# Kernel optimization log

Measured on AMD Instinct MI355X. Metric: run time of the kernel, lower is better.

Reference implementation:

```python
import jax, jax.numpy as jnp
import numpy as np

H = 16          # query heads
KV = 8          # kv heads
D = 256         # head_dim
HID = 3584      # hidden_size
ROPE_BASE = 10000.0
SCALING = 256.0 ** -0.5          # query_pre_attn_scalar ** -0.5
SOFTCAP = 50.0                   # attn_logit_softcapping
WINDOW = 1536 - 1                # sliding_window - 1 (layer_idx 0 is even)


def _rope_neox(x, positions):
    # x: [T, nh, D]; neox style: rotate the two halves of the head dim
    half = D // 2
    inv_freq = 1.0 / (ROPE_BASE ** (jnp.arange(0, D, 2, dtype=jnp.float32) / D))  # [half]
    freqs = positions.astype(jnp.float32)[:, None] * inv_freq[None, :]            # [T, half]
    cos = jnp.cos(freqs)[:, None, :]  # [T, 1, half]
    sin = jnp.sin(freqs)[:, None, :]
    x1, x2 = x[..., :half], x[..., half:]
    return jnp.concatenate([x1 * cos - x2 * sin, x2 * cos + x1 * sin], axis=-1)


def setup_inputs() -> dict:
    key = jax.random.key(0)
    k1, k2, k3 = jax.random.split(key, 3)
    T = 3072
    hidden_states = jax.random.normal(k1, (T, HID), dtype=jnp.float32)
    w_qkv = jax.random.normal(k2, (H * D + 2 * KV * D, HID), dtype=jnp.float32) * 0.02
    w_o = jax.random.normal(k3, (HID, H * D), dtype=jnp.float32) * 0.02
    positions = jnp.arange(T, dtype=jnp.int64)
    return {"positions": positions, "hidden_states": hidden_states,
            "w_qkv": w_qkv, "w_o": w_o}


def reference(positions, hidden_states, w_qkv, w_o):
    T = hidden_states.shape[0]
    qkv = hidden_states @ w_qkv.T                       # [T, (H+2KV)*D]
    q, k, v = jnp.split(qkv, [H * D, H * D + KV * D], axis=-1)
    q = q.reshape(T, H, D)
    k = k.reshape(T, KV, D)
    v = v.reshape(T, KV, D)
    q = _rope_neox(q, positions)
    k = _rope_neox(k, positions)
    # GQA: repeat kv heads (2 query heads per kv head)
    k = jnp.repeat(k, H // KV, axis=1)                  # [T, H, D]
    v = jnp.repeat(v, H // KV, axis=1)
    scores = jnp.einsum('thd,shd->hts', q, k) * SCALING  # [H, T, T]
    scores = SOFTCAP * jnp.tanh(scores / SOFTCAP)       # logit softcapping
    i = positions[:, None]
    j = positions[None, :]
    mask = (j <= i) & (i - j <= WINDOW)                 # causal + sliding window
    scores = jnp.where(mask[None, :, :], scores, -jnp.inf)
    probs = jax.nn.softmax(scores, axis=-1)
    attn = jnp.einsum('hts,shd->thd', probs, v).reshape(T, H * D)
    return attn @ w_o.T                                 # [T, HID]
```

## Files before the change

### kernel.cpp

```cpp
#include <hip/hip_runtime.h>
#include <math.h>

typedef unsigned short u16;
typedef __attribute__((ext_vector_type(8))) short short8;
typedef __attribute__((ext_vector_type(4))) float f32x4;
typedef __attribute__((ext_vector_type(4))) unsigned short u16x4;

#define HN 16
#define KVH 8
#define DH 256
#define HID 3584
#define T_LEN 3072
#define QKV_N 8192
#define O_N 4096
#define WIN 1535
#define SCALING 0.0625f
#define SOFTCAP 50.0f
#define KOFF 4096
#define VOFF 6144
#define PSTR 72
#define NJT 48
#define M_FIX 20.0f

__device__ __forceinline__ u16 f2bf(float f) {
  unsigned u = __float_as_uint(f);
  u += 0x7FFFu + ((u >> 16) & 1u);
  return (u16)(u >> 16);
}
__device__ __forceinline__ float bf2f(u16 b) {
  return __uint_as_float(((unsigned)b) << 16);
}

__device__ __forceinline__ void gload_lds16(const void* g, void* l) {
  __builtin_amdgcn_global_load_lds(
      (const __attribute__((address_space(1))) void*)g,
      (__attribute__((address_space(3))) void*)l, 16, 0, 0);
}

__device__ __forceinline__ f32x4 mfma_bf16(short8 a, short8 b, f32x4 c) {
  return __builtin_amdgcn_mfma_f32_16x16x32_bf16(a, b, c, 0, 0, 0);
}

#define BARX()                                  \
  do {                                          \
    __builtin_amdgcn_sched_barrier(0);          \
    __builtin_amdgcn_s_barrier();               \
    __builtin_amdgcn_sched_barrier(0);          \
  } while (0)

__global__ __launch_bounds__(256) void cvt_kernel(const float* __restrict__ in,
                                                  u16* __restrict__ out, int n) {
  int i = (blockIdx.x * 256 + threadIdx.x) * 4;
  if (i >= n) return;
  float4 v = *(const float4*)(in + i);
  u16x4 o;
  o[0] = f2bf(v.x); o[1] = f2bf(v.y); o[2] = f2bf(v.z); o[3] = f2bf(v.w);
  *(u16x4*)(out + i) = o;
}

template <int OUT_BF16>
__global__ __launch_bounds__(512, 2) void gemm8p(const u16* __restrict__ A,
                                                 const u16* __restrict__ B,
                                                 void* __restrict__ Cv,
                                                 int N, int K, int ntn, int cpx) {
  __shared__ u16 sA[2][256 * 64];
  __shared__ u16 sB[2][256 * 64];

  const int bid = blockIdx.x;
  const int wg = (bid & 7) * cpx + (bid >> 3);
  const int bm = wg / ntn, bn = wg % ntn;
  const int row0 = bm * 256, col0 = bn * 256;
  const int tid = threadIdx.x, lane = tid & 63, wid = tid >> 6;
  const int wr = wid >> 2, wc = wid & 3;
  const int NT = K >> 6;

  const int srow = lane >> 3;
  const int sg = (lane & 7) ^ srow;

  auto stage = [&](int tau, int kind) {
    if (tau >= NT) return;
    const int b = tau & 1;
    const int rbase = (kind & 1) * 128;
    const u16* src;
    u16* dst;
    if (kind >= 2) {
      src = A + (size_t)(row0 + rbase + wid * 8 + srow) * K + (size_t)tau * 64 + sg * 8;
      dst = &sA[b][(rbase + wid * 8) * 64];
    } else {
      src = B + (size_t)(col0 + rbase + wid * 8 + srow) * K + (size_t)tau * 64 + sg * 8;
      dst = &sB[b][(rbase + wid * 8) * 64];
    }
    gload_lds16(src, dst);
    gload_lds16(src + (size_t)64 * K, dst + 64 * 64);
  };

  f32x4 acc[8][4] = {};
  const int fr = lane & 15;
  const int fh = fr & 7;
  const int gk0 = (lane >> 4) ^ fh;
  const int gk1 = ((lane >> 4) + 4) ^ fh;

  stage(0, 0); stage(0, 1); stage(0, 2); stage(0, 3);
  stage(1, 0); stage(1, 1); stage(1, 2);
  __builtin_amdgcn_sched_barrier(0);
  asm volatile("s_waitcnt vmcnt(6)" ::: "memory");
  BARX();

  for (int u = 0; u < NT; ++u) {
    const int b = u & 1;
    const u16* pA = &sA[b][0];
    const u16* pB = &sB[b][0];
    short8 bf[4][2], afA[2][2], afB[2][2];

#define LDB_(ni, kk) (*(const short8*)&pB[(wc * 64 + (ni)*16 + fr) * 64 + (kk ? gk1 : gk0) * 8])
#define LDA_(mi, kk) (*(const short8*)&pA[(wr * 128 + (mi)*16 + fr) * 64 + (kk ? gk1 : gk0) * 8])
#define MFMA2(AF, mi0)                                                   \
  __builtin_amdgcn_s_setprio(1);                                        \
  _Pragma("unroll") for (int ni = 0; ni < 4; ++ni) {                    \
    acc[mi0][ni] = mfma_bf16(AF[0][0], bf[ni][0], acc[mi0][ni]);        \
    acc[mi0][ni] = mfma_bf16(AF[0][1], bf[ni][1], acc[mi0][ni]);        \
    acc[mi0 + 1][ni] = mfma_bf16(AF[1][0], bf[ni][0], acc[mi0 + 1][ni]);\
    acc[mi0 + 1][ni] = mfma_bf16(AF[1][1], bf[ni][1], acc[mi0 + 1][ni]);\
  }                                                                      \
  __builtin_amdgcn_s_setprio(0);                                        \
  asm volatile("s_waitcnt lgkmcnt(0)" ::: "memory");

#pragma unroll
    for (int ni = 0; ni < 4; ++ni) { bf[ni][0] = LDB_(ni, 0); bf[ni][1] = LDB_(ni, 1); }
    afA[0][0] = LDA_(0, 0); afA[0][1] = LDA_(0, 1);
    afA[1][0] = LDA_(1, 0); afA[1][1] = LDA_(1, 1);
    stage(u + 1, 3);
    BARX();
    MFMA2(afA, 0);
    BARX();
    afA[0][0] = LDA_(2, 0); afA[0][1] = LDA_(2, 1);
    afA[1][0] = LDA_(3, 0); afA[1][1] = LDA_(3, 1);
    stage(u + 2, 0);
    BARX();
    MFMA2(afA, 2);
    BARX();
    afA[0][0] = LDA_(4, 0); afA[0][1] = LDA_(4, 1);
    afA[1][0] = LDA_(5, 0); afA[1][1] = LDA_(5, 1);
    afB[0][0] = LDA_(6, 0); afB[0][1] = LDA_(6, 1);
    afB[1][0] = LDA_(7, 0); afB[1][1] = LDA_(7, 1);
    stage(u + 2, 1);
    BARX();
    MFMA2(afA, 4);
    BARX();
    stage(u + 2, 2);
    __builtin_amdgcn_sched_barrier(0);
    if (u + 2 < NT) {
      asm volatile("s_waitcnt vmcnt(6)" ::: "memory");
    } else {
      asm volatile("s_waitcnt vmcnt(0)" ::: "memory");
    }
    BARX();
    MFMA2(afB, 6);
    BARX();
#undef LDB_
#undef LDA_
#undef MFMA2
  }

#pragma unroll
  for (int mi = 0; mi < 8; ++mi) {
#pragma unroll
    for (int ni = 0; ni < 4; ++ni) {
      const int r = row0 + wr * 128 + mi * 16 + (lane >> 4) * 4;
      const int c = col0 + wc * 64 + ni * 16 + (lane & 15);
#pragma unroll
      for (int j = 0; j < 4; ++j) {
        float v = acc[mi][ni][j];
        if (OUT_BF16)
          ((u16*)Cv)[(size_t)(r + j) * N + c] = f2bf(v);
        else
          ((float*)Cv)[(size_t)(r + j) * N + c] = v;
      }
    }
  }
}

__global__ __launch_bounds__(256) void rope_kernel(u16* __restrict__ qkv) {
  int idx = blockIdx.x * 256 + threadIdx.x;
  int d = idx & 127;
  int hh = (idx >> 7) % 24;
  int t = idx / (24 * 128);
  if (t >= T_LEN) return;
  size_t base = (size_t)t * QKV_N + (hh < HN ? hh * DH : HN * DH + (hh - HN) * DH);
  float inv = exp2f((float)d * (-13.287712379549449f / 128.0f));
  float ang = (float)t * inv;
  float s = sinf(ang), c = cosf(ang);
  float x1 = bf2f(qkv[base + d]);
  float x2 = bf2f(qkv[base + d + 128]);
  qkv[base + d] = f2bf(x1 * c - x2 * s);
  qkv[base + d + 128] = f2bf(x2 * c + x1 * s);
}

__global__ __launch_bounds__(256) void vtrans_kernel(const u16* __restrict__ qkv,
                                                     u16* __restrict__ vt) {
  __shared__ u16 tile[256 * 72];
  const int jb = blockIdx.x * 64;
  const int kvh = blockIdx.y;
  const int tid = threadIdx.x;
  const int t = tid & 63, dc = tid >> 6;

  const u16* src = qkv + (size_t)(jb + t) * QKV_N + VOFF + kvh * DH + dc * 64;
#pragma unroll
  for (int i = 0; i < 8; ++i) {
    short8 v = *(const short8*)(src + i * 8);
    int d0 = dc * 64 + i * 8;
#pragma unroll
    for (int j = 0; j < 8; ++j) tile[(d0 + j) * 72 + t] = (u16)(short)v[j];
  }
  __syncthreads();

  u16* dst = vt + ((size_t)kvh * NJT + blockIdx.x) * 16384;
#pragma unroll
  for (int s = 0; s < 8; ++s) {
    int G = s * 256 + tid;
    int d = G >> 3, g = G & 7;
    short8 x = *(const short8*)&tile[d * 72 + ((g ^ (d & 7)) * 8)];
    *(short8*)(dst + G * 8) = x;
  }
}

__global__ __launch_bounds__(256) void attn_kernel(const u16* __restrict__ qkv,
                                                   const u16* __restrict__ vt,
                                                   u16* __restrict__ po,
                                                   float* __restrict__ ml) {
  const int wg = blockIdx.x;
  const int kvh = wg & 7;
  const int rest = wg >> 3;
  const int qt = rest >> 2;
  const int c = (rest >> 1) & 1;
  const int h = kvh * 2 + (rest & 1);
  const int qb = qt * 64;
  const int tid = threadIdx.x, lane = tid & 63, w = tid >> 6;

  __shared__ u16 sK[64 * 256];
  __shared__ u16 sVt[64 * 256];
  __shared__ u16 sP[4][16 * PSTR];

  int jmin = qb - WIN; if (jmin < 0) jmin = 0;
  const int jt0 = jmin >> 6, jt1 = qb >> 6;
  const int nt = jt1 - jt0 + 1;
  const int half = (nt + 1) >> 1;
  const int t_beg = (c == 0) ? jt0 : jt0 + half;
  const int t_end = (c == 0) ? jt0 + half : jt1 + 1;

  const int qrow = qb + w * 16 + (lane & 15);
  short8 qf[8];
  {
    const u16* qp = qkv + (size_t)qrow * QKV_N + h * DH + (lane >> 4) * 8;
#pragma unroll
    for (int kc = 0; kc < 8; ++kc) qf[kc] = *(const short8*)(qp + kc * 32);
  }

  f32x4 O[16];
#pragma unroll
  for (int i = 0; i < 16; ++i) O[i] = f32x4{0.f, 0.f, 0.f, 0.f};
  float lrow[4] = {0.f, 0.f, 0.f, 0.f};

  const int dl = lane & 15;
  const int vb0 = dl * 64 + (((lane >> 4)) ^ (dl & 7)) * 8;
  const int vb1 = dl * 64 + (((lane >> 4) + 4) ^ (dl & 7)) * 8;

  for (int jt = t_beg; jt < t_end; ++jt) {
    const int jb = jt * 64;
#pragma unroll
    for (int i = 0; i < 8; ++i) {
      int rl = w * 16 + i * 2 + (lane >> 5);
      int g = (lane & 31) ^ (rl & 7);
      gload_lds16(qkv + (size_t)(jb + rl) * QKV_N + KOFF + kvh * DH + g * 8,
                  &sK[(w * 16 + i * 2) * 256]);
    }
    {
      const u16* vtile = vt + ((size_t)kvh * NJT + jt) * 16384;
#pragma unroll
      for (int s = 0; s < 8; ++s) {
        int id = w * 8 + s;
        gload_lds16(vtile + id * 512 + lane * 8, &sVt[id * 512]);
      }
    }
    __syncthreads();

    f32x4 S[4];
#pragma unroll
    for (int nf = 0; nf < 4; ++nf) S[nf] = f32x4{0.f, 0.f, 0.f, 0.f};
#pragma unroll
    for (int nf = 0; nf < 4; ++nf) {
      int krow = nf * 16 + (lane & 15);
#pragma unroll
      for (int kc = 0; kc < 8; ++kc) {
        int g = (kc * 4 + (lane >> 4)) ^ (krow & 7);
        short8 kf = *(const short8*)&sK[krow * 256 + g * 8];
        S[nf] = mfma_bf16(qf[kc], kf, S[nf]);
      }
    }

#pragma unroll
    for (int r = 0; r < 4; ++r) {
      const int irow = qb + w * 16 + (lane >> 4) * 4 + r;
      const int ql = (lane >> 4) * 4 + r;
#pragma unroll
      for (int nf = 0; nf < 4; ++nf) {
        int j = jb + nf * 16 + (lane & 15);
        float x = S[nf][r] * (SCALING / SOFTCAP);
        float e2 = __expf(-2.0f * fabsf(x));
        float th = (1.0f - e2) / (1.0f + e2);
        th = x >= 0.0f ? th : -th;
        float val = SOFTCAP * th;
        bool ok = (j <= irow) && (irow - j <= WIN);
        float p = ok ? __expf(val - M_FIX) : 0.0f;
        lrow[r] += p;
        sP[w][ql * PSTR + nf * 16 + (lane & 15)] = f2bf(p);
      }
    }

    short8 pf0 = *(const short8*)&sP[w][(lane & 15) * PSTR + (lane >> 4) * 8];
    short8 pf1 = *(const short8*)&sP[w][(lane & 15) * PSTR + 32 + (lane >> 4) * 8];
#pragma unroll
    for (int nf = 0; nf < 16; ++nf) {
      short8 vf0 = *(const short8*)&sVt[nf * 1024 + vb0];
      short8 vf1 = *(const short8*)&sVt[nf * 1024 + vb1];
      O[nf] = mfma_bf16(pf0, vf0, O[nf]);
      O[nf] = mfma_bf16(pf1, vf1, O[nf]);
    }
    __syncthreads();
  }

#pragma unroll
  for (int r = 0; r < 4; ++r) {
#pragma unroll
    for (int off = 8; off >= 1; off >>= 1) lrow[r] += __shfl_xor(lrow[r], off);
  }

#pragma unroll
  for (int nf = 0; nf < 16; ++nf) {
    int d = nf * 16 + (lane & 15);
#pragma unroll
    for (int r = 0; r < 4; ++r) {
      int trow = qb + w * 16 + (lane >> 4) * 4 + r;
      po[(((size_t)c * T_LEN + trow) * HN + h) * DH + d] = f2bf(O[nf][r]);
    }
  }
  if ((lane & 15) == 0) {
#pragma unroll
    for (int r = 0; r < 4; ++r) {
      int trow = qb + w * 16 + (lane >> 4) * 4 + r;
      size_t mi = (((size_t)c * T_LEN + trow) * HN + h) * 2;
      ml[mi] = M_FIX;
      ml[mi + 1] = lrow[r];
    }
  }
}

__global__ __launch_bounds__(256) void combine_kernel(const u16* __restrict__ po,
                                                      const float* __restrict__ ml,
                                                      u16* __restrict__ attnb) {
  const int t = blockIdx.x;
  const int h = threadIdx.x >> 4;
  const int d0 = (threadIdx.x & 15) * 16;
  const size_t row = (size_t)t * HN + h;
  const float l0 = ml[row * 2 + 1];
  const float l1 = ml[(size_t)T_LEN * HN * 2 + row * 2 + 1];
  const float inv = 1.0f / (l0 + l1);
  const size_t i0 = row * DH + d0;
  const size_t i1 = (size_t)T_LEN * HN * DH + i0;
#pragma unroll
  for (int half = 0; half < 2; ++half) {
    short8 x0 = *(const short8*)(po + i0 + half * 8);
    short8 x1 = *(const short8*)(po + i1 + half * 8);
    short8 o;
#pragma unroll
    for (int j = 0; j < 8; ++j)
      o[j] = (short)f2bf((bf2f((u16)x0[j]) + bf2f((u16)x1[j])) * inv);
    *(short8*)(attnb + i0 + half * 8) = o;
  }
}

extern "C" void kernel_launch(void* const* d_in, const int* in_sizes, int n_in,
                              void* d_out, int out_size, void* d_ws, size_t ws_size,
                              hipStream_t stream) {
  const float* hidden = (const float*)d_in[1];
  const float* w_qkv = (const float*)d_in[2];
  const float* w_o = (const float*)d_in[3];
  float* out = (float*)d_out;
  char* ws = (char*)d_ws;

  u16* wqkvb = (u16*)(ws);
  u16* po = (u16*)(ws);
  float* ml = (float*)(ws + 50331648);
  u16* attnb = (u16*)(ws);
  u16* hb = (u16*)(ws + 58720256);
  u16* vtb = (u16*)(ws + 58720256);
  u16* qkvb = (u16*)(ws + 80740352);
  u16* wob = (u16*)(ws + 80740352);

  {
    int n = T_LEN * HID;
    cvt_kernel<<<dim3((n / 4 + 255) / 256), 256, 0, stream>>>(hidden, hb, n);
  }
  {
    int n = QKV_N * HID;
    cvt_kernel<<<dim3((n / 4 + 255) / 256), 256, 0, stream>>>(w_qkv, wqkvb, n);
  }
  gemm8p<1><<<dim3(384), 512, 0, stream>>>(hb, wqkvb, qkvb, QKV_N, HID, 32, 48);
  {
    int n = T_LEN * 24 * 128;
    rope_kernel<<<dim3(n / 256), 256, 0, stream>>>(qkvb);
  }
  vtrans_kernel<<<dim3(NJT, KVH), 256, 0, stream>>>(qkvb, vtb);
  attn_kernel<<<dim3(1536), 256, 0, stream>>>(qkvb, vtb, po, ml);
  {
    int n = HID * O_N;
    cvt_kernel<<<dim3((n / 4 + 255) / 256), 256, 0, stream>>>(w_o, wob, n);
  }
  combine_kernel<<<dim3(T_LEN), 256, 0, stream>>>(po, ml, attnb);
  gemm8p<0><<<dim3(168), 512, 0, stream>>>(attnb, wob, out, HID, O_N, 14, 21);
}
```

Baseline: 555.4 us.

## Use 32x32x16 MFMA GEMM for output projection and precompute RoPE cos/sin table

Adds a new gemm32 kernel that uses 32x32x16 bf16 MFMA instructions with a 256x256 tile, double-buffered LDS and an interleaved load/compute schedule, and uses it for the final output projection instead of gemm8p. The larger MFMA shape is meant to raise matrix throughput and cut LDS fragment reads per FLOP. RoPE now reads cos/sin from a table built once per call instead of computing sin/cos per element for all 24 heads. The table kernel adds a launch and workspace traffic, and the new GEMM relies on tile sizes dividing the problem.

Result: no change. 563.4 us (+1.4%).

```diff
diff --git a/kernel.cpp b/kernel.cpp
--- a/kernel.cpp
+++ b/kernel.cpp
@@ -4,6 +4,7 @@
 typedef unsigned short u16;
 typedef __attribute__((ext_vector_type(8))) short short8;
 typedef __attribute__((ext_vector_type(4))) float f32x4;
+typedef __attribute__((ext_vector_type(16))) float f32x16;
 typedef __attribute__((ext_vector_type(4))) unsigned short u16x4;
 
 #define HN 16
@@ -40,6 +41,9 @@
 __device__ __forceinline__ f32x4 mfma_bf16(short8 a, short8 b, f32x4 c) {
   return __builtin_amdgcn_mfma_f32_16x16x32_bf16(a, b, c, 0, 0, 0);
 }
+__device__ __forceinline__ f32x16 mfma32_bf16(short8 a, short8 b, f32x16 c) {
+  return __builtin_amdgcn_mfma_f32_32x32x16_bf16(a, b, c, 0, 0, 0);
+}
 
 #define BARX()                                  \
   do {                                          \
@@ -180,20 +184,148 @@
   }
 }
 
-__global__ __launch_bounds__(256) void rope_kernel(u16* __restrict__ qkv) {
+__global__ __launch_bounds__(512, 2) void gemm32(const u16* __restrict__ A,
+                                                 const u16* __restrict__ B,
+                                                 float* __restrict__ C,
+                                                 int N, int K, int ntn, int cpx) {
+  __shared__ u16 sA[2][256 * 64];
+  __shared__ u16 sB[2][256 * 64];
+
+  const int bid = blockIdx.x;
+  const int wg = (bid & 7) * cpx + (bid >> 3);
+  const int bm = wg / ntn, bn = wg % ntn;
+  const int row0 = bm * 256, col0 = bn * 256;
+  const int tid = threadIdx.x, lane = tid & 63, wid = tid >> 6;
+  const int wr = wid >> 2, wc = wid & 3;
+  const int NT = K >> 6;
+
+  const int srow = lane >> 3;
+  const int sg = (lane & 7) ^ srow;
+
+  auto stage = [&](int tau, int kind) {
+    if (tau >= NT) return;
+    const int b = tau & 1;
+    const int rbase = (kind & 1) * 128;
+    const u16* src;
+    u16* dst;
+    if (kind >= 2) {
+      src = A + (size_t)(row0 + rbase + wid * 8 + srow) * K + (size_t)tau * 64 + sg * 8;
+      dst = &sA[b][(rbase + wid * 8) * 64];
+    } else {
+      src = B + (size_t)(col0 + rbase + wid * 8 + srow) * K + (size_t)tau * 64 + sg * 8;
+      dst = &sB[b][(rbase + wid * 8) * 64];
+    }
+    gload_lds16(src, dst);
+    gload_lds16(src + (size_t)64 * K, dst + 64 * 64);
+  };
+
+  f32x16 acc[4][2] = {};
+  const int fr32 = lane & 31;
+  int gk32[4];
+#pragma unroll
+  for (int kk = 0; kk < 4; ++kk) gk32[kk] = ((kk << 1) | (lane >> 5)) ^ (fr32 & 7);
+
+  stage(0, 0); stage(0, 1); stage(0, 2); stage(0, 3);
+  stage(1, 0); stage(1, 1); stage(1, 2);
+  __builtin_amdgcn_sched_barrier(0);
+  asm volatile("s_waitcnt vmcnt(6)" ::: "memory");
+  BARX();
+
+  for (int u = 0; u < NT; ++u) {
+    const int b = u & 1;
+    const u16* pA = &sA[b][0];
+    const u16* pB = &sB[b][0];
+    short8 bf[2][4], afA[4], afB[4];
+
+#define LDB32_(nt, kk) (*(const short8*)&pB[(wc * 64 + (nt)*32 + fr32) * 64 + gk32[kk] * 8])
+#define LDA32_(mt, kk) (*(const short8*)&pA[(wr * 128 + (mt)*32 + fr32) * 64 + gk32[kk] * 8])
+#define MFMA32X(AF, mt)                                                  \
+  __builtin_amdgcn_s_setprio(1);                                        \
+  _Pragma("unroll") for (int nt = 0; nt < 2; ++nt) {                    \
+    _Pragma("unroll") for (int kk = 0; kk < 4; ++kk)                    \
+      acc[mt][nt] = mfma32_bf16(AF[kk], bf[nt][kk], acc[mt][nt]);       \
+  }                                                                      \
+  __builtin_amdgcn_s_setprio(0);                                        \
+  asm volatile("s_waitcnt lgkmcnt(0)" ::: "memory");
+
+#pragma unroll
+    for (int nt = 0; nt < 2; ++nt)
+#pragma unroll
+      for (int kk = 0; kk < 4; ++kk) bf[nt][kk] = LDB32_(nt, kk);
+#pragma unroll
+    for (int kk = 0; kk < 4; ++kk) afA[kk] = LDA32_(0, kk);
+    stage(u + 1, 3);
+    BARX();
+    MFMA32X(afA, 0);
+    BARX();
+#pragma unroll
+    for (int kk = 0; kk < 4; ++kk) afA[kk] = LDA32_(1, kk);
+    stage(u + 2, 0);
+    BARX();
+    MFMA32X(afA, 1);
+    BARX();
+#pragma unroll
+    for (int kk = 0; kk < 4; ++kk) afA[kk] = LDA32_(2, kk);
+#pragma unroll
+    for (int kk = 0; kk < 4; ++kk) afB[kk] = LDA32_(3, kk);
+    stage(u + 2, 1);
+    BARX();
+    MFMA32X(afA, 2);
+    BARX();
+    stage(u + 2, 2);
+    __builtin_amdgcn_sched_barrier(0);
+    if (u + 2 < NT) {
+      asm volatile("s_waitcnt vmcnt(6)" ::: "memory");
+    } else {
+      asm volatile("s_waitcnt vmcnt(0)" ::: "memory");
+    }
+    BARX();
+    MFMA32X(afB, 3);
+    BARX();
+#undef LDB32_
+#undef LDA32_
+#undef MFMA32X
+  }
+
+#pragma unroll
+  for (int mt = 0; mt < 4; ++mt) {
+#pragma unroll
+    for (int nt = 0; nt < 2; ++nt) {
+      const int c = col0 + wc * 64 + nt * 32 + fr32;
+#pragma unroll
+      for (int reg = 0; reg < 16; ++reg) {
+        const int r = row0 + wr * 128 + mt * 32 + (reg & 3) + 8 * (reg >> 2) + 4 * (lane >> 5);
+        C[(size_t)r * N + c] = acc[mt][nt][reg];
+      }
+    }
+  }
+}
+
+__global__ __launch_bounds__(256) void rope_table_kernel(float* __restrict__ tab) {
+  int idx = blockIdx.x * 256 + threadIdx.x;
+  int d = idx & 127;
+  int t = idx >> 7;
+  float inv = exp2f((float)d * (-13.287712379549449f / 128.0f));
+  float ang = (float)t * inv;
+  float2 cs;
+  cs.x = cosf(ang);
+  cs.y = sinf(ang);
+  *(float2*)(tab + idx * 2) = cs;
+}
+
+__global__ __launch_bounds__(256) void rope_kernel(u16* __restrict__ qkv,
+                                                   const float* __restrict__ tab) {
   int idx = blockIdx.x * 256 + threadIdx.x;
   int d = idx & 127;
   int hh = (idx >> 7) % 24;
   int t = idx / (24 * 128);
   if (t >= T_LEN) return;
   size_t base = (size_t)t * QKV_N + (hh < HN ? hh * DH : HN * DH + (hh - HN) * DH);
-  float inv = exp2f((float)d * (-13.287712379549449f / 128.0f));
-  float ang = (float)t * inv;
-  float s = sinf(ang), c = cosf(ang);
+  float2 cs = *(const float2*)(tab + ((size_t)(t << 7) + d) * 2);
   float x1 = bf2f(qkv[base + d]);
   float x2 = bf2f(qkv[base + d + 128]);
-  qkv[base + d] = f2bf(x1 * c - x2 * s);
-  qkv[base + d + 128] = f2bf(x2 * c + x1 * s);
+  qkv[base + d] = f2bf(x1 * cs.x - x2 * cs.y);
+  qkv[base + d + 128] = f2bf(x2 * cs.x + x1 * cs.y);
 }
 
 __global__ __launch_bounds__(256) void vtrans_kernel(const u16* __restrict__ qkv,
@@ -394,6 +526,7 @@
   u16* attnb = (u16*)(ws);
   u16* hb = (u16*)(ws + 58720256);
   u16* vtb = (u16*)(ws + 58720256);
+  float* ropetab = (float*)(ws + 71303168);
   u16* qkvb = (u16*)(ws + 80740352);
   u16* wob = (u16*)(ws + 80740352);
 
@@ -406,9 +539,10 @@
     cvt_kernel<<<dim3((n / 4 + 255) / 256), 256, 0, stream>>>(w_qkv, wqkvb, n);
   }
   gemm8p<1><<<dim3(384), 512, 0, stream>>>(hb, wqkvb, qkvb, QKV_N, HID, 32, 48);
+  rope_table_kernel<<<dim3(T_LEN * 128 / 256), 256, 0, stream>>>(ropetab);
   {
     int n = T_LEN * 24 * 128;
-    rope_kernel<<<dim3(n / 256), 256, 0, stream>>>(qkvb);
+    rope_kernel<<<dim3(n / 256), 256, 0, stream>>>(qkvb, ropetab);
   }
   vtrans_kernel<<<dim3(NJT, KVH), 256, 0, stream>>>(qkvb, vtb);
   attn_kernel<<<dim3(1536), 256, 0, stream>>>(qkvb, vtb, po, ml);
@@ -417,5 +551,5 @@
     cvt_kernel<<<dim3((n / 4 + 255) / 256), 256, 0, stream>>>(w_o, wob, n);
   }
   combine_kernel<<<dim3(T_LEN), 256, 0, stream>>>(po, ml, attnb);
-  gemm8p<0><<<dim3(168), 512, 0, stream>>>(attnb, wob, out, HID, O_N, 14, 21);
-}
+  gemm32<<<dim3(168), 512, 0, stream>>>(attnb, wob, out, HID, O_N, 14, 21);
+}
```

## Merge conversion kernels and precompute RoPE table in spare GEMM blocks

Applied to the files above, without the earlier changes.

Merges the hidden-state and QKV-weight fp32-to-bf16 conversions into one launch. It also folds the w_o conversion into the combine kernel and adds 128 extra blocks to the QKV GEMM launch that build a cos/sin table for RoPE, stored temporarily in the output buffer. The rope kernel then reads that table instead of calling sin/cos itself. This cuts launch count and transcendental work, at the cost of extra table traffic and heavier combine blocks. The combine kernel also gains a multiply by 1.0 that does nothing.

Result: faster. 534.3 us (-3.8%).

```diff
diff --git a/kernel.cpp b/kernel.cpp
--- a/kernel.cpp
+++ b/kernel.cpp
@@ -48,29 +48,61 @@
     __builtin_amdgcn_sched_barrier(0);          \
   } while (0)
 
-__global__ __launch_bounds__(256) void cvt_kernel(const float* __restrict__ in,
-                                                  u16* __restrict__ out, int n) {
-  int i = (blockIdx.x * 256 + threadIdx.x) * 4;
-  if (i >= n) return;
-  float4 v = *(const float4*)(in + i);
+__global__ __launch_bounds__(256) void cvt2_kernel(const float* __restrict__ a,
+                                                   u16* __restrict__ da, int nva,
+                                                   const float* __restrict__ b,
+                                                   u16* __restrict__ db, int nvb) {
+  int v = blockIdx.x * 256 + threadIdx.x;
+  const float* src;
+  u16* dst;
+  if (v < nva) {
+    src = a + (size_t)v * 4;
+    dst = da + (size_t)v * 4;
+  } else if (v < nva + nvb) {
+    int u = v - nva;
+    src = b + (size_t)u * 4;
+    dst = db + (size_t)u * 4;
+  } else {
+    return;
+  }
+  float4 x = *(const float4*)src;
   u16x4 o;
-  o[0] = f2bf(v.x); o[1] = f2bf(v.y); o[2] = f2bf(v.z); o[3] = f2bf(v.w);
-  *(u16x4*)(out + i) = o;
+  o[0] = f2bf(x.x); o[1] = f2bf(x.y); o[2] = f2bf(x.z); o[3] = f2bf(x.w);
+  *(u16x4*)dst = o;
 }
 
 template <int OUT_BF16>
 __global__ __launch_bounds__(512, 2) void gemm8p(const u16* __restrict__ A,
                                                  const u16* __restrict__ B,
                                                  void* __restrict__ Cv,
-                                                 int N, int K, int ntn, int cpx) {
+                                                 int N, int K, int ntn, int cpx,
+                                                 int gemmBlocks,
+                                                 float* __restrict__ rtab) {
   __shared__ u16 sA[2][256 * 64];
   __shared__ u16 sB[2][256 * 64];
 
   const int bid = blockIdx.x;
+  const int tid = threadIdx.x;
+
+  if (bid >= gemmBlocks) {
+    const int rb = bid - gemmBlocks;
+    for (int idx = rb * 512 + tid; idx < T_LEN * 128; idx += 128 * 512) {
+      int d = idx & 127;
+      int t = idx >> 7;
+      float inv = exp2f((float)d * (-13.287712379549449f / 128.0f));
+      float ang = (float)t * inv;
+      float2 cs;
+      cs.x = cosf(ang);
+      cs.y = sinf(ang);
+      *(float2*)(rtab + (size_t)idx * 2) = cs;
+    }
+    return;
+  }
+
   const int wg = (bid & 7) * cpx + (bid >> 3);
   const int bm = wg / ntn, bn = wg % ntn;
   const int row0 = bm * 256, col0 = bn * 256;
-  const int tid = threadIdx.x, lane = tid & 63, wid = tid >> 6;
+  const int lane = tid & 63, wid = tid >> 6;
   const int wr = wid >> 2, wc = wid & 3;
   const int NT = K >> 6;
 
@@ -180,20 +212,19 @@
   }
 }
 
-__global__ __launch_bounds__(256) void rope_kernel(u16* __restrict__ qkv) {
+__global__ __launch_bounds__(256) void rope_kernel(u16* __restrict__ qkv,
+                                                   const float* __restrict__ tab) {
   int idx = blockIdx.x * 256 + threadIdx.x;
   int d = idx & 127;
   int hh = (idx >> 7) % 24;
   int t = idx / (24 * 128);
   if (t >= T_LEN) return;
   size_t base = (size_t)t * QKV_N + (hh < HN ? hh * DH : HN * DH + (hh - HN) * DH);
-  float inv = exp2f((float)d * (-13.287712379549449f / 128.0f));
-  float ang = (float)t * inv;
-  float s = sinf(ang), c = cosf(ang);
+  float2 cs = *(const float2*)(tab + ((size_t)(t << 7) + d) * 2);
   float x1 = bf2f(qkv[base + d]);
   float x2 = bf2f(qkv[base + d + 128]);
-  qkv[base + d] = f2bf(x1 * c - x2 * s);
-  qkv[base + d + 128] = f2bf(x2 * c + x1 * s);
+  qkv[base + d] = f2bf(x1 * cs.x - x2 * cs.y);
+  qkv[base + d + 128] = f2bf(x2 * cs.x + x1 * cs.y);
 }
 
 __global__ __launch_bounds__(256) void vtrans_kernel(const u16* __restrict__ qkv,
@@ -357,7 +388,9 @@
 
 __global__ __launch_bounds__(256) void combine_kernel(const u16* __restrict__ po,
                                                       const float* __restrict__ ml,
-                                                      u16* __restrict__ attnb) {
+                                                      u16* __restrict__ attnb,
+                                                      const float* __restrict__ wo,
+                                                      u16* __restrict__ wob) {
   const int t = blockIdx.x;
   const int h = threadIdx.x >> 4;
   const int d0 = (threadIdx.x & 15) * 16;
@@ -374,8 +407,16 @@
     short8 o;
 #pragma unroll
     for (int j = 0; j < 8; ++j)
-      o[j] = (short)f2bf((bf2f((u16)x0[j]) + bf2f((u16)x1[j])) * inv);
+      o[j] = (short)f2bf((bf2f((u16)x0[j]) * bf2f((u16)0x3F80) + bf2f((u16)x1[j])) * inv);
     *(short8*)(attnb + i0 + half * 8) = o;
+  }
+
+  const int nv = (HID * O_N) / 4;
+  for (int v = blockIdx.x * 256 + threadIdx.x; v < nv; v += T_LEN * 256) {
+    float4 x = *(const float4*)(wo + (size_t)v * 4);
+    u16x4 o;
+    o[0] = f2bf(x.x); o[1] = f2bf(x.y); o[2] = f2bf(x.z); o[3] = f2bf(x.w);
+    *(u16x4*)(wob + (size_t)v * 4) = o;
   }
 }
 
@@ -396,26 +437,23 @@
   u16* vtb = (u16*)(ws + 58720256);
   u16* qkvb = (u16*)(ws + 80740352);
   u16* wob = (u16*)(ws + 80740352);
+  float* ropetab = out;
 
   {
-    int n = T_LEN * HID;
-    cvt_kernel<<<dim3((n / 4 + 255) / 256), 256, 0, stream>>>(hidden, hb, n);
-  }
-  {
-    int n = QKV_N * HID;
-    cvt_kernel<<<dim3((n / 4 + 255) / 256), 256, 0, stream>>>(w_qkv, wqkvb, n);
-  }
-  gemm8p<1><<<dim3(384), 512, 0, stream>>>(hb, wqkvb, qkvb, QKV_N, HID, 32, 48);
+    int nva = T_LEN * HID / 4;
+    int nvb = QKV_N * HID / 4;
+    cvt2_kernel<<<dim3((nva + nvb + 255) / 256), 256, 0, stream>>>(
+        hidden, hb, nva, w_qkv, wqkvb, nvb);
+  }
+  gemm8p<1><<<dim3(512), 512, 0, stream>>>(hb, wqkvb, qkvb, QKV_N, HID, 32, 48,
+                                           384, ropetab);
   {
     int n = T_LEN * 24 * 128;
-    rope_kernel<<<dim3(n / 256), 256, 0, stream>>>(qkvb);
+    rope_kernel<<<dim3(n / 256), 256, 0, stream>>>(qkvb, ropetab);
   }
   vtrans_kernel<<<dim3(NJT, KVH), 256, 0, stream>>>(qkvb, vtb);
   attn_kernel<<<dim3(1536), 256, 0, stream>>>(qkvb, vtb, po, ml);
-  {
-    int n = HID * O_N;
-    cvt_kernel<<<dim3((n / 4 + 255) / 256), 256, 0, stream>>>(w_o, wob, n);
-  }
-  combine_kernel<<<dim3(T_LEN), 256, 0, stream>>>(po, ml, attnb);
-  gemm8p<0><<<dim3(168), 512, 0, stream>>>(attnb, wob, out, HID, O_N, 14, 21);
-}
+  combine_kernel<<<dim3(T_LEN), 256, 0, stream>>>(po, ml, attnb, w_o, wob);
+  gemm8p<0><<<dim3(168), 512, 0, stream>>>(attnb, wob, out, HID, O_N, 14, 21,
+                                           168, nullptr);
+}
```
